# Optimization experiments

Hardware: AMD Instinct MI355X
Metric: run time of the kernel (lower is better)

## Reference

```python
import jax, jax.numpy as jnp
import numpy as np

H = 16
D_MODEL = 1024
D_K = D_MODEL // H
NWORDS = 16384


def setup_inputs() -> dict:
    key0 = jax.random.key(0)
    ks = jax.random.split(key0, 11)
    s = 0.02
    return {
        "query": jax.random.normal(ks[0], (1, D_MODEL), dtype=jnp.float32),
        "key": jax.random.normal(ks[1], (NWORDS, D_MODEL), dtype=jnp.float32),
        "value": jax.random.normal(ks[2], (NWORDS, D_MODEL), dtype=jnp.float32),
        "Wq": jax.random.normal(ks[3], (D_MODEL, D_MODEL), dtype=jnp.float32) * s,
        "bq": jax.random.normal(ks[4], (D_MODEL,), dtype=jnp.float32) * s,
        "Wk": jax.random.normal(ks[5], (D_MODEL, D_MODEL), dtype=jnp.float32) * s,
        "bk": jax.random.normal(ks[6], (D_MODEL,), dtype=jnp.float32) * s,
        "Wv": jax.random.normal(ks[7], (D_MODEL, D_MODEL), dtype=jnp.float32) * s,
        "bv": jax.random.normal(ks[8], (D_MODEL,), dtype=jnp.float32) * s,
        "Wo": jax.random.normal(ks[9], (D_MODEL, D_MODEL), dtype=jnp.float32) * s,
        "bo": jax.random.normal(ks[10], (D_MODEL,), dtype=jnp.float32) * s,
    }


def reference(query, key, value, Wq, bq, Wk, bk, Wv, bv, Wo, bo):
    # torch Linear: y = x @ W.T + b
    q = (query @ Wq.T + bq).reshape(H, D_K)          # [h, d_k]  (single query token)
    k = (key @ Wk.T + bk).reshape(-1, H, D_K)        # [n, h, d_k]
    v = (value @ Wv.T + bv).reshape(-1, H, D_K)      # [n, h, d_k]
    # NOTE: original module applies NO 1/sqrt(d_k) scaling.
    scores = jnp.einsum("hd,nhd->hn", q, k)          # [h, n]
    p_attn = jax.nn.softmax(scores, axis=-1)          # dropout p=0 -> no-op
    x = jnp.einsum("hn,nhd->hd", p_attn, v).reshape(1, H * D_K)  # [1, d_model]
    return x @ Wo.T + bo                              # [1, d_model]
```

## Files before the change

### kernel.cpp

```cpp
#include <hip/hip_runtime.h>

#define DM 1024
#define NW 16384

#define OFF_C    1024
#define OFF_D0   17408
#define OFF_S    17424
#define OFF_X    17696
#define OFF_W    18720
#define OFF_E    36864
#define OFF_PART 299008

__global__ __launch_bounds__(256) void k_rowdot(const float* __restrict__ W,
                                                const float* __restrict__ v,
                                                const float* __restrict__ b,
                                                float* __restrict__ out) {
  const int wave = (blockIdx.x * 256 + threadIdx.x) >> 6;
  const int lane = threadIdx.x & 63;
  const float* row = W + (size_t)wave * DM + 4 * lane;
  float s = 0.f;
#pragma unroll
  for (int j = 0; j < 4; ++j) {
    float4 a = *(const float4*)(row + j * 256);
    float4 x = *(const float4*)(v + j * 256 + 4 * lane);
    s += a.x * x.x + a.y * x.y + a.z * x.z + a.w * x.w;
  }
#pragma unroll
  for (int off = 32; off; off >>= 1) s += __shfl_xor(s, off, 64);
  if (lane == 0) out[wave] = s + b[wave];
}

__global__ __launch_bounds__(256) void k_qck(const float* __restrict__ Wq,
                                             const float* __restrict__ bq,
                                             const float* __restrict__ query,
                                             const float* __restrict__ Wk,
                                             const float* __restrict__ bk,
                                             float* __restrict__ c,
                                             float* __restrict__ d0,
                                             float* __restrict__ S) {
  const int h = blockIdx.x >> 2;
  const int mc = blockIdx.x & 3;
  const int t = threadIdx.x;
  const int lane = t & 63;
  const int wv = t >> 6;
  __shared__ float qh[64];
  if (blockIdx.x == 0 && t < 16) S[t * 16] = 0.f;
  float4 qv[4];
#pragma unroll
  for (int j = 0; j < 4; ++j) qv[j] = *(const float4*)(query + j * 256 + 4 * lane);
#pragma unroll 1
  for (int i = 0; i < 16; ++i) {
    const int d = 4 * i + wv;
    const int R = h * 64 + d;
    const float* row = Wq + (size_t)R * DM + 4 * lane;
    float s = 0.f;
#pragma unroll
    for (int j = 0; j < 4; ++j) {
      float4 a = *(const float4*)(row + j * 256);
      s += a.x * qv[j].x + a.y * qv[j].y + a.z * qv[j].z + a.w * qv[j].w;
    }
#pragma unroll
    for (int off = 32; off; off >>= 1) s += __shfl_xor(s, off, 64);
    if (lane == 0) qh[d] = s + bq[R];
  }
  __syncthreads();
  const int m = mc * 256 + t;
  const float* Wp = Wk + (size_t)(h * 64) * DM + m;
  float s = 0.f;
#pragma unroll 8
  for (int d = 0; d < 64; ++d) s += qh[d] * Wp[(size_t)d * DM];
  c[h * DM + m] = s;
  if (mc == 0 && t == 0) {
    float tt = 0.f;
    for (int d = 0; d < 64; ++d) tt += qh[d] * bk[h * 64 + d];
    d0[h] = tt;
  }
}

__global__ __launch_bounds__(256, 3) void k_scores(const float* __restrict__ key,
                                                   const float* __restrict__ c,
                                                   const float* __restrict__ d0,
                                                   float* __restrict__ e,
                                                   float* __restrict__ S) {
  const int lane = threadIdx.x & 63;
  const int wv = threadIdx.x >> 6;
  const int hbase = wv * 4;
  const int n0 = blockIdx.x * 16;
  float4 cf[4][4];
#pragma unroll
  for (int hh = 0; hh < 4; ++hh)
#pragma unroll
    for (int j = 0; j < 4; ++j)
      cf[hh][j] = *(const float4*)(c + (size_t)(hbase + hh) * DM + j * 256 + 4 * lane);
  const int hl = (lane >> 4) & 3;
  const float dh = d0[hbase + hl];
  const bool hi5 = (lane & 32) != 0;
  const bool hi4 = (lane & 16) != 0;
  const bool writer = (lane & 15) == 0;
  float Ssum = 0.f;
  for (int r = 0; r < 16; ++r) {
    const int n = n0 + r;
    const float* kp = key + (size_t)n * DM + 4 * lane;
    float4 k0 = *(const float4*)(kp + 0);
    float4 k1 = *(const float4*)(kp + 256);
    float4 k2 = *(const float4*)(kp + 512);
    float4 k3 = *(const float4*)(kp + 768);
    float s[4];
#pragma unroll
    for (int hh = 0; hh < 4; ++hh) {
      s[hh] = cf[hh][0].x * k0.x + cf[hh][0].y * k0.y + cf[hh][0].z * k0.z + cf[hh][0].w * k0.w
            + cf[hh][1].x * k1.x + cf[hh][1].y * k1.y + cf[hh][1].z * k1.z + cf[hh][1].w * k1.w
            + cf[hh][2].x * k2.x + cf[hh][2].y * k2.y + cf[hh][2].z * k2.z + cf[hh][2].w * k2.w
            + cf[hh][3].x * k3.x + cf[hh][3].y * k3.y + cf[hh][3].z * k3.z + cf[hh][3].w * k3.w;
    }
    float keep0 = hi5 ? s[2] : s[0], send0 = hi5 ? s[0] : s[2];
    float v0 = keep0 + __shfl_xor(send0, 32, 64);
    float keep1 = hi5 ? s[3] : s[1], send1 = hi5 ? s[1] : s[3];
    float v1 = keep1 + __shfl_xor(send1, 32, 64);
    float keep = hi4 ? v1 : v0, send = hi4 ? v0 : v1;
    float t = keep + __shfl_xor(send, 16, 64);
    t += __shfl_xor(t, 8, 64);
    t += __shfl_xor(t, 4, 64);
    t += __shfl_xor(t, 2, 64);
    t += __shfl_xor(t, 1, 64);
    t = __expf(t + dh);
    if (writer) {
      e[(size_t)n * 16 + hbase + hl] = t;
      Ssum += t;
    }
  }
  if (writer) atomicAdd(S + (size_t)(hbase + hl) * 16, Ssum);
}

__global__ __launch_bounds__(256, 2) void k_pv(const float* __restrict__ value,
                                               const float* __restrict__ e,
                                               float* __restrict__ part) {
  const int nb = blockIdx.x >> 2;
  const int mc = blockIdx.x & 3;
  const int lane = threadIdx.x & 63;
  const int wy = threadIdx.x >> 6;
  const int col = mc * 256 + lane * 4;
  const int n0 = nb * 128 + wy * 32;
  __shared__ float4 red[2][16][64];
  float4 acc[16];
#pragma unroll
  for (int h = 0; h < 16; ++h) acc[h] = make_float4(0.f, 0.f, 0.f, 0.f);
  const float* vp = value + (size_t)n0 * DM + col;
  const float* ep = e + (size_t)n0 * 16;
#pragma unroll 4
  for (int r = 0; r < 32; ++r) {
    float4 v = *(const float4*)(vp + (size_t)r * DM);
    const float* __restrict__ er = ep + r * 16;
#pragma unroll
    for (int h = 0; h < 16; ++h) {
      float p = er[h];
      acc[h].x = fmaf(p, v.x, acc[h].x);
      acc[h].y = fmaf(p, v.y, acc[h].y);
      acc[h].z = fmaf(p, v.z, acc[h].z);
      acc[h].w = fmaf(p, v.w, acc[h].w);
    }
  }
  if (wy >= 2) {
#pragma unroll
    for (int h = 0; h < 16; ++h) red[wy - 2][h][lane] = acc[h];
  }
  __syncthreads();
  if (wy < 2) {
#pragma unroll
    for (int h = 0; h < 16; ++h) {
      float4 o = red[wy][h][lane];
      acc[h].x += o.x; acc[h].y += o.y; acc[h].z += o.z; acc[h].w += o.w;
    }
  }
  __syncthreads();
  if (wy == 1) {
#pragma unroll
    for (int h = 0; h < 16; ++h) red[0][h][lane] = acc[h];
  }
  __syncthreads();
  if (wy == 0) {
    float* pp = part + (size_t)nb * (16 * DM) + col;
#pragma unroll
    for (int h = 0; h < 16; ++h) {
      float4 o = red[0][h][lane];
      acc[h].x += o.x; acc[h].y += o.y; acc[h].z += o.z; acc[h].w += o.w;
      *(float4*)(pp + (size_t)h * DM) = acc[h];
    }
  }
}

__global__ __launch_bounds__(256) void k_wred(const float* __restrict__ part,
                                              float* __restrict__ w) {
  const int gid = blockIdx.x * 256 + threadIdx.x;
  const int o = gid >> 2;
  const int q = gid & 3;
  float s = 0.f;
#pragma unroll 8
  for (int i = 0; i < 32; ++i) s += part[(size_t)(q * 32 + i) * 16384 + o];
  s += __shfl_xor(s, 1, 64);
  s += __shfl_xor(s, 2, 64);
  if (q == 0) w[o] = s;
}

__global__ __launch_bounds__(256) void k_xproj(const float* __restrict__ Wv,
                                               const float* __restrict__ w,
                                               const float* __restrict__ bv,
                                               const float* __restrict__ S,
                                               float* __restrict__ x) {
  const int wave = (blockIdx.x * 256 + threadIdx.x) >> 6;
  const int lane = threadIdx.x & 63;
  const int h = wave >> 6;
  const float* vec = w + (size_t)h * DM;
  const float* row = Wv + (size_t)wave * DM + 4 * lane;
  float s = 0.f;
#pragma unroll
  for (int j = 0; j < 4; ++j) {
    float4 a = *(const float4*)(row + j * 256);
    float4 x4 = *(const float4*)(vec + j * 256 + 4 * lane);
    s += a.x * x4.x + a.y * x4.y + a.z * x4.z + a.w * x4.w;
  }
#pragma unroll
  for (int off = 32; off; off >>= 1) s += __shfl_xor(s, off, 64);
  if (lane == 0) x[wave] = s / S[(size_t)h * 16] + bv[wave];
}

extern "C" void kernel_launch(void* const* d_in, const int* in_sizes, int n_in,
                              void* d_out, int out_size, void* d_ws, size_t ws_size,
                              hipStream_t stream) {
  const float* query = (const float*)d_in[0];
  const float* key   = (const float*)d_in[1];
  const float* value = (const float*)d_in[2];
  const float* Wq    = (const float*)d_in[3];
  const float* bq    = (const float*)d_in[4];
  const float* Wk    = (const float*)d_in[5];
  const float* bk    = (const float*)d_in[6];
  const float* Wv    = (const float*)d_in[7];
  const float* bv    = (const float*)d_in[8];
  const float* Wo    = (const float*)d_in[9];
  const float* bo    = (const float*)d_in[10];
  float* out = (float*)d_out;
  float* ws  = (float*)d_ws;

  k_qck    <<<64,  256, 0, stream>>>(Wq, bq, query, Wk, bk, ws + OFF_C, ws + OFF_D0, ws + OFF_S);
  k_scores <<<1024,256, 0, stream>>>(key, ws + OFF_C, ws + OFF_D0, ws + OFF_E, ws + OFF_S);
  k_pv     <<<512, 256, 0, stream>>>(value, ws + OFF_E, ws + OFF_PART);
  k_wred   <<<256, 256, 0, stream>>>(ws + OFF_PART, ws + OFF_W);
  k_xproj  <<<256, 256, 0, stream>>>(Wv, ws + OFF_W, bv, ws + OFF_S, ws + OFF_X);
  k_rowdot <<<256, 256, 0, stream>>>(Wo, ws + OFF_X, bo, out);
}
```

Before: 259.9 us.

## Batch loads ahead of use in all kernels and stage softmax weights in LDS

Several kernels are restructured to issue groups of independent global loads before consuming them: two Wq rows at a time in the q/c projection, eight Wk rows per batch, software double-buffered key rows in the score kernel, eight value rows per batch in the PV kernel, and eight partial sums per batch in the reduction. The PV kernel also stages the block's exp-score tile in shared memory and reads it as float4, replacing scalar global loads. The aim is more memory-level parallelism in these bandwidth-bound streaming loops. The cost is higher register pressure, which could reduce occupancy, especially in k_scores with its prefetch buffers.

```diff
diff --git a/kernel.cpp b/kernel.cpp
--- a/kernel.cpp
+++ b/kernel.cpp
@@ -49,26 +49,39 @@
 #pragma unroll
   for (int j = 0; j < 4; ++j) qv[j] = *(const float4*)(query + j * 256 + 4 * lane);
 #pragma unroll 1
-  for (int i = 0; i < 16; ++i) {
-    const int d = 4 * i + wv;
-    const int R = h * 64 + d;
-    const float* row = Wq + (size_t)R * DM + 4 * lane;
-    float s = 0.f;
+  for (int i = 0; i < 16; i += 2) {
+    const int d0i = 4 * i + wv;
+    const int d1i = 4 * (i + 1) + wv;
+    const float* r0 = Wq + (size_t)(h * 64 + d0i) * DM + 4 * lane;
+    const float* r1 = Wq + (size_t)(h * 64 + d1i) * DM + 4 * lane;
+    float4 a0[4], a1[4];
+#pragma unroll
+    for (int j = 0; j < 4; ++j) { a0[j] = *(const float4*)(r0 + j * 256);
+                                  a1[j] = *(const float4*)(r1 + j * 256); }
+    float s0 = 0.f, s1 = 0.f;
 #pragma unroll
     for (int j = 0; j < 4; ++j) {
-      float4 a = *(const float4*)(row + j * 256);
-      s += a.x * qv[j].x + a.y * qv[j].y + a.z * qv[j].z + a.w * qv[j].w;
-    }
-#pragma unroll
-    for (int off = 32; off; off >>= 1) s += __shfl_xor(s, off, 64);
-    if (lane == 0) qh[d] = s + bq[R];
+      s0 += a0[j].x * qv[j].x + a0[j].y * qv[j].y + a0[j].z * qv[j].z + a0[j].w * qv[j].w;
+      s1 += a1[j].x * qv[j].x + a1[j].y * qv[j].y + a1[j].z * qv[j].z + a1[j].w * qv[j].w;
+    }
+#pragma unroll
+    for (int off = 32; off; off >>= 1) { s0 += __shfl_xor(s0, off, 64);
+                                         s1 += __shfl_xor(s1, off, 64); }
+    if (lane == 0) { qh[d0i] = s0 + bq[h * 64 + d0i];
+                     qh[d1i] = s1 + bq[h * 64 + d1i]; }
   }
   __syncthreads();
   const int m = mc * 256 + t;
   const float* Wp = Wk + (size_t)(h * 64) * DM + m;
   float s = 0.f;
-#pragma unroll 8
-  for (int d = 0; d < 64; ++d) s += qh[d] * Wp[(size_t)d * DM];
+#pragma unroll 1
+  for (int db = 0; db < 8; ++db) {
+    float wv8[8];
+#pragma unroll
+    for (int j = 0; j < 8; ++j) wv8[j] = Wp[(size_t)(db * 8 + j) * DM];
+#pragma unroll
+    for (int j = 0; j < 8; ++j) s = fmaf(qh[db * 8 + j], wv8[j], s);
+  }
   c[h * DM + m] = s;
   if (mc == 0 && t == 0) {
     float tt = 0.f;
@@ -98,36 +111,55 @@
   const bool hi4 = (lane & 16) != 0;
   const bool writer = (lane & 15) == 0;
   float Ssum = 0.f;
-  for (int r = 0; r < 16; ++r) {
-    const int n = n0 + r;
-    const float* kp = key + (size_t)n * DM + 4 * lane;
-    float4 k0 = *(const float4*)(kp + 0);
-    float4 k1 = *(const float4*)(kp + 256);
-    float4 k2 = *(const float4*)(kp + 512);
-    float4 k3 = *(const float4*)(kp + 768);
-    float s[4];
-#pragma unroll
-    for (int hh = 0; hh < 4; ++hh) {
-      s[hh] = cf[hh][0].x * k0.x + cf[hh][0].y * k0.y + cf[hh][0].z * k0.z + cf[hh][0].w * k0.w
-            + cf[hh][1].x * k1.x + cf[hh][1].y * k1.y + cf[hh][1].z * k1.z + cf[hh][1].w * k1.w
-            + cf[hh][2].x * k2.x + cf[hh][2].y * k2.y + cf[hh][2].z * k2.z + cf[hh][2].w * k2.w
-            + cf[hh][3].x * k3.x + cf[hh][3].y * k3.y + cf[hh][3].z * k3.z + cf[hh][3].w * k3.w;
-    }
-    float keep0 = hi5 ? s[2] : s[0], send0 = hi5 ? s[0] : s[2];
-    float v0 = keep0 + __shfl_xor(send0, 32, 64);
-    float keep1 = hi5 ? s[3] : s[1], send1 = hi5 ? s[1] : s[3];
-    float v1 = keep1 + __shfl_xor(send1, 32, 64);
-    float keep = hi4 ? v1 : v0, send = hi4 ? v0 : v1;
-    float t = keep + __shfl_xor(send, 16, 64);
-    t += __shfl_xor(t, 8, 64);
-    t += __shfl_xor(t, 4, 64);
-    t += __shfl_xor(t, 2, 64);
-    t += __shfl_xor(t, 1, 64);
-    t = __expf(t + dh);
-    if (writer) {
-      e[(size_t)n * 16 + hbase + hl] = t;
-      Ssum += t;
-    }
+  const float* kbase = key + (size_t)n0 * DM + 4 * lane;
+  float4 kb[2][4];
+#pragma unroll
+  for (int j = 0; j < 4; ++j) {
+    kb[0][j] = *(const float4*)(kbase + j * 256);
+    kb[1][j] = *(const float4*)(kbase + DM + j * 256);
+  }
+#pragma unroll
+  for (int rr = 0; rr < 8; ++rr) {
+    float4 kn[2][4];
+    if (rr < 7) {
+      const float* kp = kbase + (size_t)(2 * rr + 2) * DM;
+#pragma unroll
+      for (int j = 0; j < 4; ++j) {
+        kn[0][j] = *(const float4*)(kp + j * 256);
+        kn[1][j] = *(const float4*)(kp + DM + j * 256);
+      }
+    }
+#pragma unroll
+    for (int b = 0; b < 2; ++b) {
+      const int n = n0 + 2 * rr + b;
+      float s[4];
+#pragma unroll
+      for (int hh = 0; hh < 4; ++hh) {
+        s[hh] = cf[hh][0].x * kb[b][0].x + cf[hh][0].y * kb[b][0].y + cf[hh][0].z * kb[b][0].z + cf[hh][0].w * kb[b][0].w
+              + cf[hh][1].x * kb[b][1].x + cf[hh][1].y * kb[b][1].y + cf[hh][1].z * kb[b][1].z + cf[hh][1].w * kb[b][1].w
+              + cf[hh][2].x * kb[b][2].x + cf[hh][2].y * kb[b][2].y + cf[hh][2].z * kb[b][2].z + cf[hh][2].w * kb[b][2].w
+              + cf[hh][3].x * kb[b][3].x + cf[hh][3].y * kb[b][3].y + cf[hh][3].z * kb[b][3].z + cf[hh][3].w * kb[b][3].w;
+      }
+      float keep0 = hi5 ? s[2] : s[0], send0 = hi5 ? s[0] : s[2];
+      float v0 = keep0 + __shfl_xor(send0, 32, 64);
+      float keep1 = hi5 ? s[3] : s[1], send1 = hi5 ? s[1] : s[3];
+      float v1 = keep1 + __shfl_xor(send1, 32, 64);
+      float keep = hi4 ? v1 : v0, send = hi4 ? v0 : v1;
+      float t = keep + __shfl_xor(send, 16, 64);
+      t += __shfl_xor(t, 8, 64);
+      t += __shfl_xor(t, 4, 64);
+      t += __shfl_xor(t, 2, 64);
+      t += __shfl_xor(t, 1, 64);
+      t = __expf(t + dh);
+      if (writer) {
+        e[(size_t)n * 16 + hbase + hl] = t;
+        Ssum += t;
+      }
+    }
+#pragma unroll
+    for (int b = 0; b < 2; ++b)
+#pragma unroll
+      for (int j = 0; j < 4; ++j) kb[b][j] = kn[b][j];
   }
   if (writer) atomicAdd(S + (size_t)(hbase + hl) * 16, Ssum);
 }
@@ -137,27 +169,42 @@
                                                float* __restrict__ part) {
   const int nb = blockIdx.x >> 2;
   const int mc = blockIdx.x & 3;
-  const int lane = threadIdx.x & 63;
-  const int wy = threadIdx.x >> 6;
+  const int t = threadIdx.x;
+  const int lane = t & 63;
+  const int wy = t >> 6;
   const int col = mc * 256 + lane * 4;
-  const int n0 = nb * 128 + wy * 32;
+  const int n0 = nb * 128;
+  __shared__ float el[128 * 16];
   __shared__ float4 red[2][16][64];
+  {
+    const float4* eg = (const float4*)(e + (size_t)n0 * 16);
+    float4* es = (float4*)el;
+    es[t] = eg[t];
+    es[t + 256] = eg[t + 256];
+  }
+  __syncthreads();
   float4 acc[16];
 #pragma unroll
   for (int h = 0; h < 16; ++h) acc[h] = make_float4(0.f, 0.f, 0.f, 0.f);
-  const float* vp = value + (size_t)n0 * DM + col;
-  const float* ep = e + (size_t)n0 * 16;
-#pragma unroll 4
-  for (int r = 0; r < 32; ++r) {
-    float4 v = *(const float4*)(vp + (size_t)r * DM);
-    const float* __restrict__ er = ep + r * 16;
-#pragma unroll
-    for (int h = 0; h < 16; ++h) {
-      float p = er[h];
-      acc[h].x = fmaf(p, v.x, acc[h].x);
-      acc[h].y = fmaf(p, v.y, acc[h].y);
-      acc[h].z = fmaf(p, v.z, acc[h].z);
-      acc[h].w = fmaf(p, v.w, acc[h].w);
+  const float* vp = value + (size_t)(n0 + wy * 32) * DM + col;
+  const float* ep = &el[wy * 32 * 16];
+#pragma unroll 1
+  for (int rb = 0; rb < 4; ++rb) {
+    float4 v[8];
+#pragma unroll
+    for (int i = 0; i < 8; ++i) v[i] = *(const float4*)(vp + (size_t)(rb * 8 + i) * DM);
+#pragma unroll
+    for (int i = 0; i < 8; ++i) {
+      const float4* er4 = (const float4*)(ep + (rb * 8 + i) * 16);
+      float4 e0 = er4[0], e1 = er4[1], e2 = er4[2], e3 = er4[3];
+      float4 vv = v[i];
+#define FMA4H(H, P) { acc[H].x = fmaf(P, vv.x, acc[H].x); acc[H].y = fmaf(P, vv.y, acc[H].y); \
+                      acc[H].z = fmaf(P, vv.z, acc[H].z); acc[H].w = fmaf(P, vv.w, acc[H].w); }
+      FMA4H(0,  e0.x) FMA4H(1,  e0.y) FMA4H(2,  e0.z) FMA4H(3,  e0.w)
+      FMA4H(4,  e1.x) FMA4H(5,  e1.y) FMA4H(6,  e1.z) FMA4H(7,  e1.w)
+      FMA4H(8,  e2.x) FMA4H(9,  e2.y) FMA4H(10, e2.z) FMA4H(11, e2.w)
+      FMA4H(12, e3.x) FMA4H(13, e3.y) FMA4H(14, e3.z) FMA4H(15, e3.w)
+#undef FMA4H
     }
   }
   if (wy >= 2) {
@@ -195,8 +242,14 @@
   const int o = gid >> 2;
   const int q = gid & 3;
   float s = 0.f;
-#pragma unroll 8
-  for (int i = 0; i < 32; ++i) s += part[(size_t)(q * 32 + i) * 16384 + o];
+#pragma unroll 1
+  for (int ib = 0; ib < 4; ++ib) {
+    float x[8];
+#pragma unroll
+    for (int j = 0; j < 8; ++j) x[j] = part[(size_t)(q * 32 + ib * 8 + j) * 16384 + o];
+#pragma unroll
+    for (int j = 0; j < 8; ++j) s += x[j];
+  }
   s += __shfl_xor(s, 1, 64);
   s += __shfl_xor(s, 2, 64);
   if (q == 0) w[o] = s;
```

Measured after the change: 240.3 us. 7.5% less time.
